# Performance work log

Measured on AMD Instinct MI355X. Metric: run time of the kernel, lower is better.

## Reference

```python
import jax, jax.numpy as jnp
import numpy as np

B, NP, NFFT, SPACING = 4096, 512, 4096, 8


def setup_inputs() -> dict:
    key = jax.random.key(0)
    LS_ri = jax.random.normal(key, (B, NP, 2), dtype=jnp.float32)  # real/imag of LS_est
    # 1-based comb pilot positions: 1, 9, ..., 4089 (sorted, min == 1)
    pilot_pos = 1.0 + SPACING * jnp.arange(NP, dtype=jnp.float32)
    # nn.Parameter init: log(exp(initial_decay) - 1), initial_decay = 0.5
    decay_param = jnp.array([np.log(np.exp(0.5) - 1.0)], dtype=jnp.float32)
    return {"LS_ri": LS_ri, "pilot_pos": pilot_pos, "decay_param": decay_param, "Nfft": NFFT}


def reference(LS_ri, pilot_pos, decay_param, Nfft):
    # decay = softplus(raw param)
    decay = jax.nn.softplus(decay_param[0])
    # torch code: if min(pilot_loc) == 1 -> shift to 0-based (true by construction)
    loc = pilot_pos - 1.0                                  # [NP], 0-based pilot locations
    H = LS_ri                                              # [B, NP, 2]

    # pilot_loc[0] > 0 branch: linearly extrapolate a pilot at subcarrier 0
    slope_l = (H[:, 1] - H[:, 0]) / (loc[1] - loc[0])      # [B, 2]
    h0 = H[:, 0] - slope_l * loc[0]
    # pilot_loc[-1] < Nfft-1 branch: extrapolate a pilot at subcarrier Nfft-1
    slope_r = (H[:, -1] - H[:, -2]) / (loc[-1] - loc[-2])
    hN = H[:, -1] + slope_r * (Nfft - 1 - loc[-1])

    H = jnp.concatenate([h0[:, None], H, hN[:, None]], axis=1)           # [B, NP+2, 2]
    loc = jnp.concatenate([jnp.zeros((1,), loc.dtype), loc,
                           jnp.full((1,), Nfft - 1, loc.dtype)])          # [NP+2]

    i = jnp.arange(Nfft, dtype=loc.dtype)                                 # [Nfft]
    left = jnp.clip(jnp.searchsorted(loc, i, side='right') - 1, 0, loc.shape[0] - 2)
    right = left + 1
    x0, x1 = loc[left], loc[right]                                        # [Nfft]
    y0, y1 = H[:, left], H[:, right]                                      # [B, Nfft, 2]

    w_l = jnp.exp(-decay * jnp.abs(i - x0))                               # [Nfft]
    w_r = jnp.exp(-decay * jnp.abs(x1 - i))
    w = (w_l + w_r + 1e-12)
    out = (w_l[None, :, None] * y0 + w_r[None, :, None] * y1) / w[None, :, None]
    return out  # [B, Nfft, 2] (real/imag of complex estimate)
```

## Files before the change

### kernel.cpp

```cpp
#include <hip/hip_runtime.h>


#define NP_MAX 512

__global__ void dai_weights_kernel(const float* __restrict__ pilot_pos,
                                   const float* __restrict__ decay_param,
                                   float4* __restrict__ wout,
                                   int NP, int Nfft) {
    int i = blockIdx.x * blockDim.x + threadIdx.x;
    if (i >= Nfft) return;

    float decay = log1pf(expf(decay_param[0]));
    float fi = (float)i;

    int lo = 0, hi = NP;
    while (lo < hi) {
        int mid = (lo + hi) >> 1;
        if (pilot_pos[mid] - 1.0f <= fi) lo = mid + 1; else hi = mid;
    }
    int count = 1 + lo + (((float)(Nfft - 1)) <= fi ? 1 : 0);
    int left = count - 1;
    left = min(max(left, 0), NP);
    int right = left + 1;

    float x0 = (left == 0) ? 0.0f
             : (left <= NP ? pilot_pos[left - 1] - 1.0f : (float)(Nfft - 1));
    float x1 = (right <= NP) ? pilot_pos[right - 1] - 1.0f : (float)(Nfft - 1);

    float wl = expf(-decay * fabsf(fi - x0));
    float wr = expf(-decay * fabsf(x1 - fi));
    float w = wl + wr + 1e-12f;

    float4 o;
    o.x = wl / w;
    o.y = wr / w;
    o.z = __int_as_float(left);
    o.w = 0.0f;
    wout[i] = o;
}

__global__ __launch_bounds__(256) void dai_interp_kernel(
        const float* __restrict__ LS,
        const float* __restrict__ pilot_pos,
        const float4* __restrict__ wts,
        float* __restrict__ out,
        int NP, int Nfft) {
    __shared__ float2 hext[NP_MAX + 2];

    const int b = blockIdx.x;
    const int t = threadIdx.x;

    {
        const float4* row4 = (const float4*)(LS + (size_t)b * NP * 2);
        const int n4 = (NP * 2) / 4;
        for (int idx = t; idx < n4; idx += 256) {
            float4 v = row4[idx];
            hext[1 + 2 * idx] = make_float2(v.x, v.y);
            hext[2 + 2 * idx] = make_float2(v.z, v.w);
        }
    }
    __syncthreads();

    if (t == 0) {
        float2 H0 = hext[1], H1 = hext[2];
        float2 Hl = hext[NP], Hll = hext[NP - 1];
        float loc0 = pilot_pos[0] - 1.0f;
        float loc1 = pilot_pos[1] - 1.0f;
        float locl = pilot_pos[NP - 1] - 1.0f;
        float locll = pilot_pos[NP - 2] - 1.0f;

        float sl = 1.0f / (loc1 - loc0);
        float2 h0;
        h0.x = H0.x - (H1.x - H0.x) * sl * loc0;
        h0.y = H0.y - (H1.y - H0.y) * sl * loc0;

        float sr = 1.0f / (locl - locll);
        float tr = (float)(Nfft - 1) - locl;
        float2 hN;
        hN.x = Hl.x + (Hl.x - Hll.x) * sr * tr;
        hN.y = Hl.y + (Hl.y - Hll.y) * sr * tr;

        hext[0] = h0;
        hext[NP + 1] = hN;
    }
    __syncthreads();

    float4* out4 = (float4*)(out + (size_t)b * Nfft * 2);
    const int npairs = Nfft >> 1;
    for (int p = t; p < npairs; p += 256) {
        float4 w0 = wts[2 * p];
        float4 w1 = wts[2 * p + 1];
        int l0 = __float_as_int(w0.z);
        int l1 = __float_as_int(w1.z);
        float2 y00 = hext[l0], y01 = hext[l0 + 1];
        float2 y10 = hext[l1], y11 = hext[l1 + 1];
        float4 o;
        o.x = w0.x * y00.x + w0.y * y01.x;
        o.y = w0.x * y00.y + w0.y * y01.y;
        o.z = w1.x * y10.x + w1.y * y11.x;
        o.w = w1.x * y10.y + w1.y * y11.y;
        out4[p] = o;
    }
}

extern "C" void kernel_launch(void* const* d_in, const int* in_sizes, int n_in,
                              void* d_out, int out_size, void* d_ws, size_t ws_size,
                              hipStream_t stream) {
    const float* LS     = (const float*)d_in[0];
    const float* pilot  = (const float*)d_in[1];
    const float* decayp = (const float*)d_in[2];

    const int NP   = in_sizes[1];
    const int B    = in_sizes[0] / (2 * NP);
    const int Nfft = out_size / (2 * B);

    float4* wts = (float4*)d_ws;

    dai_weights_kernel<<<(Nfft + 255) / 256, 256, 0, stream>>>(
        pilot, decayp, wts, NP, Nfft);
    dai_interp_kernel<<<B, 256, 0, stream>>>(
        LS, pilot, wts, (float*)d_out, NP, Nfft);
}
```

Before: 159.0 us.

## Process multiple rows per block with register-cached weights and double-buffered staging

Adds a specialized interpolation kernel for NP=512, Nfft=4096 in which each block handles four batch rows. The per-subcarrier weights are loaded into registers once and reused across those rows. The next row's pilots are staged into a second shared buffer while the current row is computed, which removes one barrier per row. A generic fallback handles other shapes, at the cost of more registers per thread and fewer blocks.

```diff
diff --git a/kernel.cpp b/kernel.cpp
--- a/kernel.cpp
+++ b/kernel.cpp
@@ -1,7 +1,10 @@
 #include <hip/hip_runtime.h>
 
 
-#define NP_MAX 512
+#define NP_C    512
+#define NFFT_C  4096
+#define ROWS_C  4
+#define THREADS 256
 
 __global__ void dai_weights_kernel(const float* __restrict__ pilot_pos,
                                    const float* __restrict__ decay_param,
@@ -19,8 +22,7 @@
         if (pilot_pos[mid] - 1.0f <= fi) lo = mid + 1; else hi = mid;
     }
     int count = 1 + lo + (((float)(Nfft - 1)) <= fi ? 1 : 0);
-    int left = count - 1;
-    left = min(max(left, 0), NP);
+    int left = min(max(count - 1, 0), NP);
     int right = left + 1;
 
     float x0 = (left == 0) ? 0.0f
@@ -39,67 +41,115 @@
     wout[i] = o;
 }
 
-__global__ __launch_bounds__(256) void dai_interp_kernel(
+__global__ __launch_bounds__(THREADS) void dai_interp_mr(
         const float* __restrict__ LS,
         const float* __restrict__ pilot_pos,
         const float4* __restrict__ wts,
-        float* __restrict__ out,
+        float* __restrict__ out) {
+    constexpr int NP = NP_C, NFFT = NFFT_C, ROWS = ROWS_C;
+    constexpr int PAIRS = NFFT / 2;
+    constexpr int PPT = PAIRS / THREADS;
+
+    __shared__ float2 hext[2][NP + 2];
+
+    const int t = threadIdx.x;
+    const int b0 = blockIdx.x * ROWS;
+
+    float4 w0[PPT], w1[PPT];
+#pragma unroll
+    for (int j = 0; j < PPT; ++j) {
+        int p = t + THREADS * j;
+        w0[j] = wts[2 * p];
+        w1[j] = wts[2 * p + 1];
+    }
+
+    const float loc0  = pilot_pos[0] - 1.0f;
+    const float loc1  = pilot_pos[1] - 1.0f;
+    const float locll = pilot_pos[NP - 2] - 1.0f;
+    const float locl  = pilot_pos[NP - 1] - 1.0f;
+    const float inv_l = 1.0f / (loc1 - loc0);
+    const float inv_r = 1.0f / (locl - locll);
+    const float tr    = (float)(NFFT - 1) - locl;
+
+    auto stage = [&](int r, int buf) {
+        const float* rowp = LS + (size_t)(b0 + r) * NP * 2;
+        float4 v = ((const float4*)rowp)[t];
+        float2* dst = hext[buf];
+        dst[1 + 2 * t] = make_float2(v.x, v.y);
+        dst[2 + 2 * t] = make_float2(v.z, v.w);
+        if (t == 0) {
+            float2 H0  = ((const float2*)rowp)[0];
+            float2 H1  = ((const float2*)rowp)[1];
+            float2 Hll = ((const float2*)rowp)[NP - 2];
+            float2 Hl  = ((const float2*)rowp)[NP - 1];
+            float2 h0, hN;
+            h0.x = H0.x - (H1.x - H0.x) * inv_l * loc0;
+            h0.y = H0.y - (H1.y - H0.y) * inv_l * loc0;
+            hN.x = Hl.x + (Hl.x - Hll.x) * inv_r * tr;
+            hN.y = Hl.y + (Hl.y - Hll.y) * inv_r * tr;
+            dst[0] = h0;
+            dst[NP + 1] = hN;
+        }
+    };
+
+    stage(0, 0);
+    __syncthreads();
+
+    for (int r = 0; r < ROWS; ++r) {
+        if (r + 1 < ROWS) stage(r + 1, (r + 1) & 1);
+
+        const float2* h = hext[r & 1];
+        float4* out4 = (float4*)(out + (size_t)(b0 + r) * NFFT * 2);
+#pragma unroll
+        for (int j = 0; j < PPT; ++j) {
+            int p = t + THREADS * j;
+            int l0 = __float_as_int(w0[j].z);
+            int l1 = __float_as_int(w1[j].z);
+            float2 y00 = h[l0], y01 = h[l0 + 1];
+            float2 y10 = h[l1], y11 = h[l1 + 1];
+            float4 o;
+            o.x = w0[j].x * y00.x + w0[j].y * y01.x;
+            o.y = w0[j].x * y00.y + w0[j].y * y01.y;
+            o.z = w1[j].x * y10.x + w1[j].y * y11.x;
+            o.w = w1[j].x * y10.y + w1[j].y * y11.y;
+            out4[p] = o;
+        }
+        __syncthreads();
+    }
+}
+
+__global__ __launch_bounds__(256) void dai_interp_generic(
+        const float* __restrict__ LS, const float* __restrict__ pilot_pos,
+        const float4* __restrict__ wts, float* __restrict__ out,
         int NP, int Nfft) {
-    __shared__ float2 hext[NP_MAX + 2];
-
+    extern __shared__ float2 hext[];
     const int b = blockIdx.x;
     const int t = threadIdx.x;
-
     {
-        const float4* row4 = (const float4*)(LS + (size_t)b * NP * 2);
-        const int n4 = (NP * 2) / 4;
-        for (int idx = t; idx < n4; idx += 256) {
-            float4 v = row4[idx];
-            hext[1 + 2 * idx] = make_float2(v.x, v.y);
-            hext[2 + 2 * idx] = make_float2(v.z, v.w);
-        }
+        const float2* row2 = (const float2*)(LS + (size_t)b * NP * 2);
+        for (int idx = t; idx < NP; idx += 256) hext[1 + idx] = row2[idx];
     }
     __syncthreads();
-
     if (t == 0) {
         float2 H0 = hext[1], H1 = hext[2];
         float2 Hl = hext[NP], Hll = hext[NP - 1];
-        float loc0 = pilot_pos[0] - 1.0f;
-        float loc1 = pilot_pos[1] - 1.0f;
-        float locl = pilot_pos[NP - 1] - 1.0f;
-        float locll = pilot_pos[NP - 2] - 1.0f;
-
-        float sl = 1.0f / (loc1 - loc0);
-        float2 h0;
-        h0.x = H0.x - (H1.x - H0.x) * sl * loc0;
-        h0.y = H0.y - (H1.y - H0.y) * sl * loc0;
-
-        float sr = 1.0f / (locl - locll);
-        float tr = (float)(Nfft - 1) - locl;
-        float2 hN;
-        hN.x = Hl.x + (Hl.x - Hll.x) * sr * tr;
-        hN.y = Hl.y + (Hl.y - Hll.y) * sr * tr;
-
-        hext[0] = h0;
-        hext[NP + 1] = hN;
+        float loc0 = pilot_pos[0] - 1.0f, loc1 = pilot_pos[1] - 1.0f;
+        float locl = pilot_pos[NP - 1] - 1.0f, locll = pilot_pos[NP - 2] - 1.0f;
+        float sl = 1.0f / (loc1 - loc0), sr = 1.0f / (locl - locll);
+        float trr = (float)(Nfft - 1) - locl;
+        hext[0] = make_float2(H0.x - (H1.x - H0.x) * sl * loc0,
+                              H0.y - (H1.y - H0.y) * sl * loc0);
+        hext[NP + 1] = make_float2(Hl.x + (Hl.x - Hll.x) * sr * trr,
+                                   Hl.y + (Hl.y - Hll.y) * sr * trr);
     }
     __syncthreads();
-
-    float4* out4 = (float4*)(out + (size_t)b * Nfft * 2);
-    const int npairs = Nfft >> 1;
-    for (int p = t; p < npairs; p += 256) {
-        float4 w0 = wts[2 * p];
-        float4 w1 = wts[2 * p + 1];
-        int l0 = __float_as_int(w0.z);
-        int l1 = __float_as_int(w1.z);
-        float2 y00 = hext[l0], y01 = hext[l0 + 1];
-        float2 y10 = hext[l1], y11 = hext[l1 + 1];
-        float4 o;
-        o.x = w0.x * y00.x + w0.y * y01.x;
-        o.y = w0.x * y00.y + w0.y * y01.y;
-        o.z = w1.x * y10.x + w1.y * y11.x;
-        o.w = w1.x * y10.y + w1.y * y11.y;
-        out4[p] = o;
+    float2* out2 = (float2*)(out + (size_t)b * Nfft * 2);
+    for (int i = t; i < Nfft; i += 256) {
+        float4 w = wts[i];
+        int l = __float_as_int(w.z);
+        float2 y0 = hext[l], y1 = hext[l + 1];
+        out2[i] = make_float2(w.x * y0.x + w.y * y1.x,
+                              w.x * y0.y + w.y * y1.y);
     }
 }
 
@@ -118,6 +168,12 @@
 
     dai_weights_kernel<<<(Nfft + 255) / 256, 256, 0, stream>>>(
         pilot, decayp, wts, NP, Nfft);
-    dai_interp_kernel<<<B, 256, 0, stream>>>(
-        LS, pilot, wts, (float*)d_out, NP, Nfft);
+
+    if (NP == NP_C && Nfft == NFFT_C && (B % ROWS_C) == 0) {
+        dai_interp_mr<<<B / ROWS_C, THREADS, 0, stream>>>(
+            LS, pilot, wts, (float*)d_out);
+    } else {
+        dai_interp_generic<<<B, 256, (NP + 2) * sizeof(float2), stream>>>(
+            LS, pilot, wts, (float*)d_out, NP, Nfft);
+    }
 }
```

Result: no change. 156.5 us (-1.6%).
